# Kernel optimization log

Measured on AMD Instinct MI355X. Metric: run time of the kernel, lower is better.

The kernel has to match this reference:

```python
import jax, jax.numpy as jnp
import numpy as np

G = (1.0, 1.0)  # Clifford signature g = [1, 1]
MODES1 = 32
MODES2 = 32


def _clifford_kernel_2d(w, g):
    # w: (4, O, Cin, 2*m1, 2*m2); returns (4*O, 4*Cin, 2*m1, 2*m2)
    g0, g1 = g
    k0 = jnp.concatenate([w[0], g0 * w[1], g1 * w[2], -g0 * g1 * w[3]], axis=1)
    k1 = jnp.concatenate([w[1], w[0], -g1 * w[3], g1 * w[2]], axis=1)
    k2 = jnp.concatenate([w[2], g0 * w[3], w[0], -g0 * w[1]], axis=1)
    k3 = jnp.concatenate([w[3], w[2], -w[1], w[0]], axis=1)
    return jnp.concatenate([k0, k1, k2, k3], axis=0)


def _forward(x, weights):
    # x: (B, C, H, W, 4) multivector field
    B, C, H, W, I = x.shape
    m1, m2 = MODES1, MODES2
    # dual-pair complexification: (scalar, e12) and (e1, e2)
    d1 = jax.lax.complex(x[..., 0], x[..., 3])
    d2 = jax.lax.complex(x[..., 1], x[..., 2])
    d1f = jnp.fft.fft2(d1)  # over last two axes (H, W)
    d2f = jnp.fft.fft2(d2)
    # stacked blades in Fourier space: (B, 4*C, H, W)
    mv = jnp.concatenate([d1f.real, d2f.real, d2f.imag, d1f.imag], axis=1)
    # crop low-frequency corner modes into a (2*m1, 2*m2) block
    top = jnp.concatenate([mv[:, :, :m1, :m2], mv[:, :, :m1, -m2:]], axis=-1)
    bot = jnp.concatenate([mv[:, :, -m1:, :m2], mv[:, :, -m1:, -m2:]], axis=-1)
    inp = jnp.concatenate([top, bot], axis=-2)  # (B, 4*C, 2*m1, 2*m2)
    kernel = _clifford_kernel_2d(weights, G)  # (4*O, 4*C, 2*m1, 2*m2)
    out = jnp.einsum('bixy,oixy->boxy', inp, kernel)  # geometric-product mode mix
    O4 = kernel.shape[0]
    # scatter the four corners back into a zero-padded full spectrum
    out_ft = jnp.zeros((B, O4, H, W), dtype=x.dtype)
    out_ft = out_ft.at[:, :, :m1, :m2].set(out[:, :, :m1, :m2])
    out_ft = out_ft.at[:, :, -m1:, :m2].set(out[:, :, -m1:, :m2])
    out_ft = out_ft.at[:, :, :m1, -m2:].set(out[:, :, :m1, -m2:])
    out_ft = out_ft.at[:, :, -m1:, -m2:].set(out[:, :, -m1:, -m2:])
    # (B, 4, O, H, W) -> (B, O, H, W, 4)
    out_ft = out_ft.reshape(B, 4, O4 // 4, H, W).transpose(0, 2, 3, 4, 1)
    od1 = jax.lax.complex(out_ft[..., 0], out_ft[..., 3])
    od2 = jax.lax.complex(out_ft[..., 1], out_ft[..., 2])
    o1 = jnp.fft.ifft2(od1)
    o2 = jnp.fft.ifft2(od2)
    return jnp.stack([o1.real, o2.real, o2.imag, o1.imag], axis=-1)


def setup_inputs() -> dict:
    key = jax.random.key(0)
    kx, kw = jax.random.split(key)
    B, Cin, Cout, H, W = 4, 32, 32, 256, 256
    x = jax.random.normal(kx, (B, Cin, H, W, 4), dtype=jnp.float32)
    scale = 1.0 / (Cin * Cout)
    weights = scale * jax.random.uniform(kw, (4, Cout, Cin, 2 * MODES1, 2 * MODES2), dtype=jnp.float32)
    return {"x": x, "weights": weights}


def reference(x, weights):
    return _forward(x, weights)
```

## Files before the change

kernel.cpp:

```cpp
#include <hip/hip_runtime.h>
#include <math.h>

#define TWO_PI 6.28318530717958647692f

__device__ __forceinline__ void cmac(float2& a, const float2 b, const float2 c) {
  a.x = fmaf(b.x, c.x, fmaf(-b.y, c.y, a.x));
  a.y = fmaf(b.x, c.y, fmaf(b.y, c.x, a.y));
}
__device__ __forceinline__ float2 cmul(const float2 a, const float2 b) {
  return make_float2(fmaf(a.x, b.x, -a.y * b.y), fmaf(a.x, b.y, a.y * b.x));
}

#define W16_C {1.f, 0.92387953f, 0.70710678f, 0.38268343f, 0.f, -0.38268343f, -0.70710678f, -0.92387953f, -1.f, -0.92387953f, -0.70710678f, -0.38268343f, 0.f, 0.38268343f, 0.70710678f, 0.92387953f}
#define W16_S {0.f, 0.38268343f, 0.70710678f, 0.92387953f, 1.f, 0.92387953f, 0.70710678f, 0.38268343f, 0.f, -0.38268343f, -0.70710678f, -0.92387953f, -1.f, -0.92387953f, -0.70710678f, -0.38268343f}

__device__ __forceinline__ void idft16_p1(const float2* a, const int p1,
                                          float2* X) {
  const float WC[16] = W16_C;
  const float WS[16] = W16_S;
  float2 tt[4];
#pragma unroll
  for (int r1 = 0; r1 < 4; ++r1) {
    const float2 q0 = a[r1], q1 = a[r1 + 4], q2 = a[r1 + 8], q3 = a[r1 + 12];
    const float2 s = make_float2(q0.x + q2.x, q0.y + q2.y);
    const float2 d = make_float2(q0.x - q2.x, q0.y - q2.y);
    const float2 u = make_float2(q1.x + q3.x, q1.y + q3.y);
    const float2 e = make_float2(q1.x - q3.x, q1.y - q3.y);
    float2 in;
    if (p1 == 0)      in = make_float2(s.x + u.x, s.y + u.y);
    else if (p1 == 1) in = make_float2(d.x - e.y, d.y + e.x);
    else if (p1 == 2) in = make_float2(s.x - u.x, s.y - u.y);
    else              in = make_float2(d.x + e.y, d.y - e.x);
    const float wc = WC[(r1 * p1) & 15], ws = WS[(r1 * p1) & 15];
    tt[r1] = make_float2(fmaf(in.x, wc, -in.y * ws), fmaf(in.y, wc, in.x * ws));
  }
  const float2 s = make_float2(tt[0].x + tt[2].x, tt[0].y + tt[2].y);
  const float2 d = make_float2(tt[0].x - tt[2].x, tt[0].y - tt[2].y);
  const float2 u = make_float2(tt[1].x + tt[3].x, tt[1].y + tt[3].y);
  const float2 e = make_float2(tt[1].x - tt[3].x, tt[1].y - tt[3].y);
  X[0] = make_float2(s.x + u.x, s.y + u.y);
  X[1] = make_float2(d.x - e.y, d.y + e.x);
  X[2] = make_float2(s.x - u.x, s.y - u.y);
  X[3] = make_float2(d.x + e.y, d.y - e.x);
}

__global__ __launch_bounds__(256) void f1_dft_h(const float* __restrict__ x,
                                                float* __restrict__ G) {
  __shared__ float2 twn[256];
  __shared__ float2 yf[64][4][2][8];
  const int t = threadIdx.x;
  {
    float sv, cv;
    sincosf(-TWO_PI * (float)t * (1.0f / 256.0f), &sv, &cv);
    twn[t] = make_float2(cv, sv);
  }
  const int bid = blockIdx.x;
  const int img = bid >> 5;
  const int w0  = (bid & 31) << 3;
  const float4* __restrict__ xb = (const float4*)x + (size_t)img * 65536 + w0;
  {
    const int wl  = t & 7;
    const int n1g = t >> 3;
#pragma unroll
    for (int ii = 0; ii < 2; ++ii) {
      const int n1 = n1g * 2 + ii;
      const float4 v0 = xb[(size_t)(n1)*256 + wl];
      const float4 v1 = xb[(size_t)(n1 + 64) * 256 + wl];
      const float4 v2 = xb[(size_t)(n1 + 128) * 256 + wl];
      const float4 v3 = xb[(size_t)(n1 + 192) * 256 + wl];
      {
        const float sx = v0.x + v2.x, sy = v0.w + v2.w;
        const float dx = v0.x - v2.x, dy = v0.w - v2.w;
        const float ux = v1.x + v3.x, uy = v1.w + v3.w;
        const float ex = v1.x - v3.x, ey = v1.w - v3.w;
        yf[n1][0][0][wl] = make_float2(sx + ux, sy + uy);
        yf[n1][2][0][wl] = make_float2(sx - ux, sy - uy);
        yf[n1][1][0][wl] = make_float2(dx + ey, dy - ex);
        yf[n1][3][0][wl] = make_float2(dx - ey, dy + ex);
      }
      {
        const float sx = v0.y + v2.y, sy = v0.z + v2.z;
        const float dx = v0.y - v2.y, dy = v0.z - v2.z;
        const float ux = v1.y + v3.y, uy = v1.z + v3.z;
        const float ex = v1.y - v3.y, ey = v1.z - v3.z;
        yf[n1][0][1][wl] = make_float2(sx + ux, sy + uy);
        yf[n1][2][1][wl] = make_float2(sx - ux, sy - uy);
        yf[n1][1][1][wl] = make_float2(dx + ey, dy - ex);
        yf[n1][3][1][wl] = make_float2(dx - ey, dy + ex);
      }
    }
  }
  __syncthreads();
  const int wl   = t & 7;
  const int dual = (t >> 3) & 1;
  const int kb   = t >> 4;
  const int r    = kb & 3;
  float2 acc[16];
#pragma unroll
  for (int c = 0; c < 16; ++c) acc[c] = make_float2(0.f, 0.f);
  int idx = 0;
#pragma unroll
  for (int n1 = 0; n1 < 64; ++n1) {
    const float2 tv = twn[idx];
    const float2 yv = yf[n1][r][dual][wl];
    cmac(acc[n1 & 15], yv, tv);
    idx = (idx + kb) & 255;
  }
  const float WC[16] = W16_C;
  const float WS[16] = W16_S;
  float2 D0 = make_float2(0.f, 0.f), D1 = D0, D2 = D0, D3 = D0;
#pragma unroll
  for (int c = 0; c < 16; ++c) {
    const float2 a = acc[c];
    const float cc = WC[c], ss = WS[c];
    const float cc2 = WC[(2 * c) & 15], ss2 = WS[(2 * c) & 15];
    D0.x += a.x;                         D0.y += a.y;
    D1.x = fmaf(a.x, cc,  fmaf( a.y, ss,  D1.x));
    D1.y = fmaf(a.y, cc,  fmaf(-a.x, ss,  D1.y));
    D2.x = fmaf(a.x, cc2, fmaf(-a.y, ss2, D2.x));
    D2.y = fmaf(a.y, cc2, fmaf( a.x, ss2, D2.y));
    D3.x = fmaf(a.x, cc,  fmaf(-a.y, ss,  D3.x));
    D3.y = fmaf(a.y, cc,  fmaf( a.x, ss,  D3.y));
  }
  float2* __restrict__ Gp = (float2*)G;
  const size_t base = ((size_t)(img * 2 + dual) * 64) * 256 + w0 + wl;
  Gp[base + (size_t)(kb)*256]      = D0;
  Gp[base + (size_t)(kb + 16)*256] = D1;
  Gp[base + (size_t)(kb + 32)*256] = D2;
  Gp[base + (size_t)(kb + 48)*256] = D3;
}

__global__ __launch_bounds__(256) void f2_dft_w(const float* __restrict__ G,
                                                float* __restrict__ mi) {
  __shared__ float2 yf[16][65][4];
  const int t = threadIdx.x;
  const int row0 = blockIdx.x * 16;
  for (int idx = t; idx < 1024; idx += 256) {
    const int tr = idx >> 6, n1 = idx & 63;
    const float2* __restrict__ Gp = (const float2*)G + (size_t)(row0 + tr) * 256;
    const float2 z0 = Gp[n1], z1 = Gp[n1 + 64], z2 = Gp[n1 + 128], z3 = Gp[n1 + 192];
    const float sx = z0.x + z2.x, sy = z0.y + z2.y;
    const float dx = z0.x - z2.x, dy = z0.y - z2.y;
    const float ux = z1.x + z3.x, uy = z1.y + z3.y;
    const float ex = z1.x - z3.x, ey = z1.y - z3.y;
    yf[tr][n1][0] = make_float2(sx + ux, sy + uy);
    yf[tr][n1][2] = make_float2(sx - ux, sy - uy);
    yf[tr][n1][1] = make_float2(dx + ey, dy - ex);
    yf[tr][n1][3] = make_float2(dx - ey, dy + ex);
  }
  __syncthreads();
  const int trow  = t >> 4;
  const int kslot = t & 15;
  const int r     = kslot & 3;
  float2 st[4], st16[4], anc[4], acc[4];
#pragma unroll
  for (int m = 0; m < 4; ++m) {
    const int ki = kslot + (m << 4);
    const float fr = (float)((ki < 32) ? ki : ki - 64);
    float sv, cv;
    sincosf(-TWO_PI * fr * (1.0f / 256.0f), &sv, &cv);
    st[m] = make_float2(cv, sv);
    sincosf(-TWO_PI * fr * (1.0f / 16.0f), &sv, &cv);
    st16[m] = make_float2(cv, sv);
    anc[m] = make_float2(1.f, 0.f);
    acc[m] = make_float2(0.f, 0.f);
  }
#pragma unroll 1
  for (int c4 = 0; c4 < 4; ++c4) {
    float2 w[4];
#pragma unroll
    for (int m = 0; m < 4; ++m) w[m] = anc[m];
#pragma unroll
    for (int tt = 0; tt < 16; ++tt) {
      const float2 yv = yf[trow][c4 * 16 + tt][r];
#pragma unroll
      for (int m = 0; m < 4; ++m) {
        cmac(acc[m], yv, w[m]);
        w[m] = cmul(w[m], st[m]);
      }
    }
#pragma unroll
    for (int m = 0; m < 4; ++m) anc[m] = cmul(anc[m], st16[m]);
  }
  const int row  = row0 + trow;
  const int kx   = row & 63;
  const int dual = (row >> 6) & 1;
  const int bc   = row >> 7;
  const int b = bc >> 5, cc = bc & 31;
  const int sRe = dual ? 1 : 0;
  const int sIm = dual ? 2 : 3;
#pragma unroll
  for (int m = 0; m < 4; ++m) {
    const int kyi = kslot + (m << 4);
    const size_t moff = (size_t)kx * 64 + kyi;
    mi[(((size_t)(b * 4 + sRe)) * 32 + cc) * 4096 + moff] = acc[m].x;
    mi[(((size_t)(b * 4 + sIm)) * 32 + cc) * 4096 + moff] = acc[m].y;
  }
}

__global__ __launch_bounds__(512) void ein_k(const float* __restrict__ mi,
                                             const float* __restrict__ wgt,
                                             float* __restrict__ mo) {
  __shared__ float si[4][128][32];
  const int t = threadIdx.x;
  const int bid = blockIdx.x;
  const int m0 = (bid >> 1) << 5;
  const int oh = bid & 1;
  for (int idx = t; idx < 16384; idx += 512) {
    const int q = idx & 31, i = (idx >> 5) & 127, b = idx >> 12;
    si[b][i][q] = mi[((size_t)b * 128 + i) * 4096 + m0 + q];
  }
  __syncthreads();
  const int q = t & 31;
  const int o = oh * 16 + (t >> 5);
  float acc[4][4];
#pragma unroll
  for (int b = 0; b < 4; ++b)
#pragma unroll
    for (int r = 0; r < 4; ++r) acc[b][r] = 0.f;
#pragma unroll 2
  for (int c = 0; c < 32; ++c) {
    float wv[4];
#pragma unroll
    for (int j = 0; j < 4; ++j)
      wv[j] = wgt[(((size_t)j * 32 + o) * 32 + c) * 4096 + m0 + q];
#pragma unroll
    for (int b = 0; b < 4; ++b) {
      const float iv0 = si[b][c][q];
      const float iv1 = si[b][32 + c][q];
      const float iv2 = si[b][64 + c][q];
      const float iv3 = si[b][96 + c][q];
      acc[b][0] += wv[0] * iv0 + wv[1] * iv1 + wv[2] * iv2 - wv[3] * iv3;
      acc[b][1] += wv[1] * iv0 + wv[0] * iv1 - wv[3] * iv2 + wv[2] * iv3;
      acc[b][2] += wv[2] * iv0 + wv[3] * iv1 + wv[0] * iv2 - wv[1] * iv3;
      acc[b][3] += wv[3] * iv0 + wv[2] * iv1 - wv[1] * iv2 + wv[0] * iv3;
    }
  }
#pragma unroll
  for (int b = 0; b < 4; ++b)
#pragma unroll
    for (int r = 0; r < 4; ++r)
      mo[(((size_t)b * 4 + r) * 32 + o) * 4096 + m0 + q] = acc[b][r];
}

__global__ __launch_bounds__(256) void i1_idft_w(const float* __restrict__ mo,
                                                 float* __restrict__ T) {
  __shared__ float2 srow[4][64];
  const int t = threadIdx.x;
  const int trow = t >> 6, lane = t & 63;
  const int row = blockIdx.x * 4 + trow;
  const int kx = row & 63;
  const int dual = (row >> 6) & 1;
  const int bo = row >> 7;
  const int b = bo >> 5, o = bo & 31;
  const int rA = dual ? 1 : 0;
  const int rB = dual ? 2 : 3;
  const size_t ibase = (size_t)kx * 64 + lane;
  srow[trow][lane] = make_float2(mo[(((size_t)b * 4 + rA) * 32 + o) * 4096 + ibase],
                                 mo[(((size_t)b * 4 + rB) * 32 + o) * 4096 + ibase]);
  __syncthreads();
  const int n1 = lane;
  float sv, cv;
  sincosf(TWO_PI * (float)n1 * (1.0f / 256.0f), &sv, &cv);
  const float2 w1 = make_float2(cv, sv);
  sincosf(TWO_PI * (float)n1 * (1.0f / 64.0f), &sv, &cv);
  const float2 step = make_float2(cv, sv);
  float2 w[4];
  w[0] = make_float2(1.f, 0.f);
  w[1] = w1;
  w[2] = cmul(w1, w1);
  w[3] = cmul(w[2], w1);
  float2 accA[4], accB[4];
#pragma unroll
  for (int r = 0; r < 4; ++r) {
    accA[r] = make_float2(0.f, 0.f);
    accB[r] = make_float2(0.f, 0.f);
  }
#pragma unroll
  for (int tt = 0; tt < 8; ++tt)
#pragma unroll
    for (int r = 0; r < 4; ++r) {
      cmac(accA[r], srow[trow][r + 4 * tt], w[r]);
      w[r] = cmul(w[r], step);
    }
#pragma unroll
  for (int tt = 8; tt < 16; ++tt)
#pragma unroll
    for (int r = 0; r < 4; ++r) {
      cmac(accB[r], srow[trow][r + 4 * tt], w[r]);
      w[r] = cmul(w[r], step);
    }
  const int qq = n1 & 3;
  const float2 rot = make_float2((float)((qq == 0) - (qq == 2)),
                                 (float)((qq == 3) - (qq == 1)));
  float2 V[4];
#pragma unroll
  for (int r = 0; r < 4; ++r) {
    const float2 Br = cmul(accB[r], rot);
    V[r] = make_float2(accA[r].x + Br.x, accA[r].y + Br.y);
  }
  const float sx = V[0].x + V[2].x, sy = V[0].y + V[2].y;
  const float dx = V[0].x - V[2].x, dy = V[0].y - V[2].y;
  const float ux = V[1].x + V[3].x, uy = V[1].y + V[3].y;
  const float ex = V[1].x - V[3].x, ey = V[1].y - V[3].y;
  float2* __restrict__ Tp = (float2*)T + (size_t)row * 256;
  Tp[n1]       = make_float2(sx + ux, sy + uy);
  Tp[n1 + 64]  = make_float2(dx - ey, dy + ex);
  Tp[n1 + 128] = make_float2(sx - ux, sy - uy);
  Tp[n1 + 192] = make_float2(dx + ey, dy - ex);
}

__global__ __launch_bounds__(256) void i2_idft_h(const float* __restrict__ T,
                                                 float* __restrict__ out) {
  __shared__ float2 twc[256];
  __shared__ float2 Tl[2][64][16];
  const int t = threadIdx.x;
  {
    float sv, cv;
    sincosf(TWO_PI * (float)t * (1.0f / 256.0f), &sv, &cv);
    twc[t] = make_float2(cv, sv);
  }
  const int bid = blockIdx.x;
  const int bo = bid >> 4;
  const int w0 = (bid & 15) << 4;
  const float2* __restrict__ Tp = (const float2*)T + (size_t)bo * 32768;
  for (int idx = t; idx < 2048; idx += 256) {
    const int ww = idx & 15, kxi = (idx >> 4) & 63, dual = idx >> 10;
    Tl[dual][kxi][ww] = Tp[((size_t)dual * 64 + kxi) * 256 + w0 + ww];
  }
  __syncthreads();
  const int wl = t & 15;
  const int n1 = t >> 4;
  float2 a0[16], a1[16];
#pragma unroll
  for (int c = 0; c < 16; ++c) {
    a0[c] = make_float2(0.f, 0.f);
    a1[c] = make_float2(0.f, 0.f);
  }
  int idx = 0;
#pragma unroll
  for (int kxi = 0; kxi < 64; ++kxi) {
    if (kxi == 32) idx = (idx + 192 * n1) & 255;
    const float2 tv = twc[idx];
    cmac(a0[kxi & 15], Tl[0][kxi][wl], tv);
    cmac(a1[kxi & 15], Tl[1][kxi][wl], tv);
    idx = (idx + n1) & 255;
  }
  const float sc = 1.0f / 65536.0f;
  float4* __restrict__ op = (float4*)out + (size_t)bo * 65536 + w0 + wl;
#pragma unroll
  for (int p1 = 0; p1 < 4; ++p1) {
    float2 X0[4], X1[4];
    idft16_p1(a0, p1, X0);
    idft16_p1(a1, p1, X1);
#pragma unroll
    for (int p2 = 0; p2 < 4; ++p2) {
      const int h = n1 + 16 * (p1 + 4 * p2);
      op[(size_t)h * 256] = make_float4(X0[p2].x * sc, X1[p2].x * sc,
                                        X1[p2].y * sc, X0[p2].y * sc);
    }
  }
}

extern "C" void kernel_launch(void* const* d_in, const int* in_sizes, int n_in,
                              void* d_out, int out_size, void* d_ws, size_t ws_size,
                              hipStream_t stream) {
  const float* x = (const float*)d_in[0];
  const float* wgt = (const float*)d_in[1];
  float* out = (float*)d_out;
  float* G  = (float*)d_ws;
  float* mi = G + 8388608;
  float* mo = mi + 2097152;

  hipLaunchKernelGGL(f1_dft_h, dim3(4096), dim3(256), 0, stream, x, G);
  hipLaunchKernelGGL(f2_dft_w, dim3(1024), dim3(256), 0, stream, G, mi);
  hipLaunchKernelGGL(ein_k,    dim3(256),  dim3(512), 0, stream, mi, wgt, mo);
  hipLaunchKernelGGL(i1_idft_w, dim3(4096), dim3(256), 0, stream, mo, G);
  hipLaunchKernelGGL(i2_idft_h, dim3(2048), dim3(256), 0, stream, G, out);
}
```

Before: 143.0 us.

## Use shared twiddle tables and 16-point decompositions in middle DFT stages, retile einsum

f2_dft_w stops generating twiddles with chained complex multiplies. It now reads them from a shared-memory table indexed by a modular counter, accumulates into 16 residue bins, and finishes with a small constant-twiddle combine. i1_idft_w is restructured the same way, handling 16 rows per block with table twiddles and the existing idft16 helper instead of recurrences. The einsum kernel uses 16-mode tiles with 256 threads and twice the blocks, and software-prefetches the next weight values. The aim is to cut serial complex-multiply dependency chains and raise parallelism, at the cost of more registers (16 accumulators) and shared-memory twiddle lookups.

```diff
diff --git a/kernel.cpp b/kernel.cpp
--- a/kernel.cpp
+++ b/kernel.cpp
@@ -6,9 +6,6 @@
 __device__ __forceinline__ void cmac(float2& a, const float2 b, const float2 c) {
   a.x = fmaf(b.x, c.x, fmaf(-b.y, c.y, a.x));
   a.y = fmaf(b.x, c.y, fmaf(b.y, c.x, a.y));
-}
-__device__ __forceinline__ float2 cmul(const float2 a, const float2 b) {
-  return make_float2(fmaf(a.x, b.x, -a.y * b.y), fmaf(a.x, b.y, a.y * b.x));
 }
 
 #define W16_C {1.f, 0.92387953f, 0.70710678f, 0.38268343f, 0.f, -0.38268343f, -0.70710678f, -0.92387953f, -1.f, -0.92387953f, -0.70710678f, -0.38268343f, 0.f, 0.38268343f, 0.70710678f, 0.92387953f}
@@ -132,8 +129,14 @@
 
 __global__ __launch_bounds__(256) void f2_dft_w(const float* __restrict__ G,
                                                 float* __restrict__ mi) {
+  __shared__ float2 twn[256];
   __shared__ float2 yf[16][65][4];
   const int t = threadIdx.x;
+  {
+    float sv, cv;
+    sincosf(-TWO_PI * (float)t * (1.0f / 256.0f), &sv, &cv);
+    twn[t] = make_float2(cv, sv);
+  }
   const int row0 = blockIdx.x * 16;
   for (int idx = t; idx < 1024; idx += 256) {
     const int tr = idx >> 6, n1 = idx & 63;
@@ -149,38 +152,36 @@
     yf[tr][n1][3] = make_float2(dx - ey, dy + ex);
   }
   __syncthreads();
+  const int kslot = t & 15;
   const int trow  = t >> 4;
-  const int kslot = t & 15;
   const int r     = kslot & 3;
-  float2 st[4], st16[4], anc[4], acc[4];
-#pragma unroll
-  for (int m = 0; m < 4; ++m) {
-    const int ki = kslot + (m << 4);
-    const float fr = (float)((ki < 32) ? ki : ki - 64);
-    float sv, cv;
-    sincosf(-TWO_PI * fr * (1.0f / 256.0f), &sv, &cv);
-    st[m] = make_float2(cv, sv);
-    sincosf(-TWO_PI * fr * (1.0f / 16.0f), &sv, &cv);
-    st16[m] = make_float2(cv, sv);
-    anc[m] = make_float2(1.f, 0.f);
-    acc[m] = make_float2(0.f, 0.f);
-  }
-#pragma unroll 1
-  for (int c4 = 0; c4 < 4; ++c4) {
-    float2 w[4];
-#pragma unroll
-    for (int m = 0; m < 4; ++m) w[m] = anc[m];
-#pragma unroll
-    for (int tt = 0; tt < 16; ++tt) {
-      const float2 yv = yf[trow][c4 * 16 + tt][r];
-#pragma unroll
-      for (int m = 0; m < 4; ++m) {
-        cmac(acc[m], yv, w[m]);
-        w[m] = cmul(w[m], st[m]);
-      }
-    }
-#pragma unroll
-    for (int m = 0; m < 4; ++m) anc[m] = cmul(anc[m], st16[m]);
+  float2 acc[16];
+#pragma unroll
+  for (int c = 0; c < 16; ++c) acc[c] = make_float2(0.f, 0.f);
+  int idx = 0;
+#pragma unroll
+  for (int n1 = 0; n1 < 64; ++n1) {
+    const float2 tv = twn[idx];
+    const float2 yv = yf[trow][n1][r];
+    cmac(acc[n1 & 15], yv, tv);
+    idx = (idx + kslot) & 255;
+  }
+  const float WC[16] = W16_C;
+  const float WS[16] = W16_S;
+  float2 D[4];
+  D[0] = make_float2(0.f, 0.f); D[1] = D[0]; D[2] = D[0]; D[3] = D[0];
+#pragma unroll
+  for (int c = 0; c < 16; ++c) {
+    const float2 a = acc[c];
+    const float cc = WC[c], ss = WS[c];
+    const float cc2 = WC[(2 * c) & 15], ss2 = WS[(2 * c) & 15];
+    D[0].x += a.x;                        D[0].y += a.y;
+    D[1].x = fmaf(a.x, cc,  fmaf( a.y, ss,  D[1].x));
+    D[1].y = fmaf(a.y, cc,  fmaf(-a.x, ss,  D[1].y));
+    D[2].x = fmaf(a.x, cc2, fmaf(-a.y, ss2, D[2].x));
+    D[2].y = fmaf(a.y, cc2, fmaf( a.x, ss2, D[2].y));
+    D[3].x = fmaf(a.x, cc,  fmaf(-a.y, ss,  D[3].x));
+    D[3].y = fmaf(a.y, cc,  fmaf( a.x, ss,  D[3].y));
   }
   const int row  = row0 + trow;
   const int kx   = row & 63;
@@ -193,37 +194,45 @@
   for (int m = 0; m < 4; ++m) {
     const int kyi = kslot + (m << 4);
     const size_t moff = (size_t)kx * 64 + kyi;
-    mi[(((size_t)(b * 4 + sRe)) * 32 + cc) * 4096 + moff] = acc[m].x;
-    mi[(((size_t)(b * 4 + sIm)) * 32 + cc) * 4096 + moff] = acc[m].y;
-  }
-}
-
-__global__ __launch_bounds__(512) void ein_k(const float* __restrict__ mi,
+    mi[(((size_t)(b * 4 + sRe)) * 32 + cc) * 4096 + moff] = D[m].x;
+    mi[(((size_t)(b * 4 + sIm)) * 32 + cc) * 4096 + moff] = D[m].y;
+  }
+}
+
+__global__ __launch_bounds__(256) void ein_k(const float* __restrict__ mi,
                                              const float* __restrict__ wgt,
                                              float* __restrict__ mo) {
-  __shared__ float si[4][128][32];
+  __shared__ float si[4][128][16];
   const int t = threadIdx.x;
   const int bid = blockIdx.x;
-  const int m0 = (bid >> 1) << 5;
+  const int m0 = (bid >> 1) << 4;
   const int oh = bid & 1;
-  for (int idx = t; idx < 16384; idx += 512) {
-    const int q = idx & 31, i = (idx >> 5) & 127, b = idx >> 12;
+  for (int idx = t; idx < 8192; idx += 256) {
+    const int q = idx & 15, i = (idx >> 4) & 127, b = idx >> 11;
     si[b][i][q] = mi[((size_t)b * 128 + i) * 4096 + m0 + q];
   }
   __syncthreads();
-  const int q = t & 31;
-  const int o = oh * 16 + (t >> 5);
+  const int q = t & 15;
+  const int o = oh * 16 + (t >> 4);
+  const float* __restrict__ wb = wgt + (size_t)o * 32 * 4096 + m0 + q;
   float acc[4][4];
 #pragma unroll
   for (int b = 0; b < 4; ++b)
 #pragma unroll
     for (int r = 0; r < 4; ++r) acc[b][r] = 0.f;
-#pragma unroll 2
+  float wn[4];
+#pragma unroll
+  for (int j = 0; j < 4; ++j) wn[j] = wb[(size_t)j * 1024 * 4096];
+#pragma unroll 1
   for (int c = 0; c < 32; ++c) {
     float wv[4];
 #pragma unroll
-    for (int j = 0; j < 4; ++j)
-      wv[j] = wgt[(((size_t)j * 32 + o) * 32 + c) * 4096 + m0 + q];
+    for (int j = 0; j < 4; ++j) wv[j] = wn[j];
+    if (c < 31) {
+#pragma unroll
+      for (int j = 0; j < 4; ++j)
+        wn[j] = wb[((size_t)j * 1024 + (c + 1)) * 4096];
+    }
 #pragma unroll
     for (int b = 0; b < 4; ++b) {
       const float iv0 = si[b][c][q];
@@ -245,69 +254,51 @@
 
 __global__ __launch_bounds__(256) void i1_idft_w(const float* __restrict__ mo,
                                                  float* __restrict__ T) {
-  __shared__ float2 srow[4][64];
-  const int t = threadIdx.x;
-  const int trow = t >> 6, lane = t & 63;
-  const int row = blockIdx.x * 4 + trow;
-  const int kx = row & 63;
-  const int dual = (row >> 6) & 1;
-  const int bo = row >> 7;
-  const int b = bo >> 5, o = bo & 31;
-  const int rA = dual ? 1 : 0;
-  const int rB = dual ? 2 : 3;
-  const size_t ibase = (size_t)kx * 64 + lane;
-  srow[trow][lane] = make_float2(mo[(((size_t)b * 4 + rA) * 32 + o) * 4096 + ibase],
-                                 mo[(((size_t)b * 4 + rB) * 32 + o) * 4096 + ibase]);
-  __syncthreads();
-  const int n1 = lane;
-  float sv, cv;
-  sincosf(TWO_PI * (float)n1 * (1.0f / 256.0f), &sv, &cv);
-  const float2 w1 = make_float2(cv, sv);
-  sincosf(TWO_PI * (float)n1 * (1.0f / 64.0f), &sv, &cv);
-  const float2 step = make_float2(cv, sv);
-  float2 w[4];
-  w[0] = make_float2(1.f, 0.f);
-  w[1] = w1;
-  w[2] = cmul(w1, w1);
-  w[3] = cmul(w[2], w1);
-  float2 accA[4], accB[4];
-#pragma unroll
-  for (int r = 0; r < 4; ++r) {
-    accA[r] = make_float2(0.f, 0.f);
-    accB[r] = make_float2(0.f, 0.f);
-  }
-#pragma unroll
-  for (int tt = 0; tt < 8; ++tt)
-#pragma unroll
-    for (int r = 0; r < 4; ++r) {
-      cmac(accA[r], srow[trow][r + 4 * tt], w[r]);
-      w[r] = cmul(w[r], step);
-    }
-#pragma unroll
-  for (int tt = 8; tt < 16; ++tt)
-#pragma unroll
-    for (int r = 0; r < 4; ++r) {
-      cmac(accB[r], srow[trow][r + 4 * tt], w[r]);
-      w[r] = cmul(w[r], step);
-    }
-  const int qq = n1 & 3;
-  const float2 rot = make_float2((float)((qq == 0) - (qq == 2)),
-                                 (float)((qq == 3) - (qq == 1)));
-  float2 V[4];
-#pragma unroll
-  for (int r = 0; r < 4; ++r) {
-    const float2 Br = cmul(accB[r], rot);
-    V[r] = make_float2(accA[r].x + Br.x, accA[r].y + Br.y);
-  }
-  const float sx = V[0].x + V[2].x, sy = V[0].y + V[2].y;
-  const float dx = V[0].x - V[2].x, dy = V[0].y - V[2].y;
-  const float ux = V[1].x + V[3].x, uy = V[1].y + V[3].y;
-  const float ex = V[1].x - V[3].x, ey = V[1].y - V[3].y;
+  __shared__ float2 twc[256];
+  __shared__ float2 srow[16][66];
+  const int t = threadIdx.x;
+  {
+    float sv, cv;
+    sincosf(TWO_PI * (float)t * (1.0f / 256.0f), &sv, &cv);
+    twc[t] = make_float2(cv, sv);
+  }
+  const int row0 = blockIdx.x * 16;
+  for (int idx = t; idx < 1024; idx += 256) {
+    const int tr = idx >> 6, ky = idx & 63;
+    const int row = row0 + tr;
+    const int kx = row & 63;
+    const int dual = (row >> 6) & 1;
+    const int bo = row >> 7;
+    const int b = bo >> 5, o = bo & 31;
+    const int rA = dual ? 1 : 0;
+    const int rB = dual ? 2 : 3;
+    const size_t ib = (size_t)kx * 64 + ky;
+    srow[tr][ky] = make_float2(mo[(((size_t)b * 4 + rA) * 32 + o) * 4096 + ib],
+                               mo[(((size_t)b * 4 + rB) * 32 + o) * 4096 + ib]);
+  }
+  __syncthreads();
+  const int n1   = t & 15;
+  const int trow = t >> 4;
+  float2 a[16];
+#pragma unroll
+  for (int c = 0; c < 16; ++c) a[c] = make_float2(0.f, 0.f);
+  int idx = 0;
+#pragma unroll
+  for (int kyi = 0; kyi < 64; ++kyi) {
+    if (kyi == 32) idx = (idx + 192 * n1) & 255;
+    cmac(a[kyi & 15], srow[trow][kyi], twc[idx]);
+    idx = (idx + n1) & 255;
+  }
+  const int row = row0 + trow;
   float2* __restrict__ Tp = (float2*)T + (size_t)row * 256;
-  Tp[n1]       = make_float2(sx + ux, sy + uy);
-  Tp[n1 + 64]  = make_float2(dx - ey, dy + ex);
-  Tp[n1 + 128] = make_float2(sx - ux, sy - uy);
-  Tp[n1 + 192] = make_float2(dx + ey, dy - ex);
+#pragma unroll
+  for (int p1 = 0; p1 < 4; ++p1) {
+    float2 X[4];
+    idft16_p1(a, p1, X);
+#pragma unroll
+    for (int p2 = 0; p2 < 4; ++p2)
+      Tp[n1 + 16 * (p1 + 4 * p2)] = X[p2];
+  }
 }
 
 __global__ __launch_bounds__(256) void i2_idft_h(const float* __restrict__ T,
@@ -374,7 +365,7 @@
 
   hipLaunchKernelGGL(f1_dft_h, dim3(4096), dim3(256), 0, stream, x, G);
   hipLaunchKernelGGL(f2_dft_w, dim3(1024), dim3(256), 0, stream, G, mi);
-  hipLaunchKernelGGL(ein_k,    dim3(256),  dim3(512), 0, stream, mi, wgt, mo);
-  hipLaunchKernelGGL(i1_idft_w, dim3(4096), dim3(256), 0, stream, mo, G);
+  hipLaunchKernelGGL(ein_k,    dim3(512),  dim3(256), 0, stream, mi, wgt, mo);
+  hipLaunchKernelGGL(i1_idft_w, dim3(1024), dim3(256), 0, stream, mo, G);
   hipLaunchKernelGGL(i2_idft_h, dim3(2048), dim3(256), 0, stream, G, out);
 }
```

New measurement: 136.4 us. -4.6%, faster.
